# Kernel optimization log

Hardware: AMD Instinct MI355X
Metric: run time of the kernel (lower is better)

## Reference

```python
import jax, jax.numpy as jnp
import numpy as np

STRIDE = 2
PADDING = (1, 1)
OUT_PADDING = (0, 0)


def conv_transpose2d(x, weight, bias, stride, padding, out_padding):
    # weight: (Cin, Cout, kh, kw) -- torch ConvTranspose2d layout.
    # The original code does: stride-insert zeros, zero-pad by (k-1), append
    # out_padding rows/cols, valid-conv with the spatially-flipped kernel,
    # then crop `padding` from each side. That is exactly a dilated conv:
    kh, kw = weight.shape[2], weight.shape[3]
    w = jnp.flip(weight, (2, 3)).transpose(1, 0, 2, 3)  # (Cout, Cin, kh, kw)
    pad = ((kh - 1 - padding[0], kh - 1 - padding[0] + out_padding[0]),
           (kw - 1 - padding[1], kw - 1 - padding[1] + out_padding[1]))
    out = jax.lax.conv_general_dilated(
        x, w,
        window_strides=(1, 1),
        padding=pad,
        lhs_dilation=(stride, stride),
        dimension_numbers=('NCHW', 'OIHW', 'NCHW'))
    return out + bias[None, :, None, None]


def setup_inputs() -> dict:
    key = jax.random.key(0)
    k1, k2, k3 = jax.random.split(key, 3)
    Cin, Cout, kh, kw = 256, 128, 4, 4
    bnd = (1.0 / (Cin * kh * kw)) ** 0.5  # matches uniform_(-k**0.5, k**0.5)
    x = jax.random.normal(k1, (16, Cin, 64, 64), dtype=jnp.float32)
    weight = jax.random.uniform(k2, (Cin, Cout, kh, kw), jnp.float32, -bnd, bnd)
    bias = jax.random.uniform(k3, (Cout,), jnp.float32, -bnd, bnd)
    return {"x": x, "weight": weight, "bias": bias}


def reference(x, weight, bias):
    # Output: (16, 128, 128, 128) = (H-1)*2 - 2*1 + 4
    return conv_transpose2d(x, weight, bias, STRIDE, PADDING, OUT_PADDING)
```

## Files before the change

### kernel.cpp

```cpp
#include <hip/hip_runtime.h>
#include <stdint.h>

typedef unsigned short u16;
typedef __bf16 bf16x8 __attribute__((ext_vector_type(8)));
typedef float f32x4 __attribute__((ext_vector_type(4)));
typedef float f32x2 __attribute__((ext_vector_type(2)));

static const size_t XT_BYTES = (size_t)16 * 66 * 66 * 256 * 2;
static const size_t WK_BYTES = (size_t)2 * 2 * 8 * 2 * 2 * 128 * 32 * 2;

__device__ __forceinline__ u16 f2bf(float f) {
  unsigned u = __float_as_uint(f);
  unsigned r = (u + 0x7fff + ((u >> 16) & 1)) >> 16;
  return (u16)r;
}

__device__ __forceinline__ void ld_g2l16(const u16* g, void* l) {
  __builtin_amdgcn_global_load_lds(
      (const __attribute__((address_space(1))) unsigned int*)(uintptr_t)g,
      (__attribute__((address_space(3))) unsigned int*)(unsigned int)(uintptr_t)l,
      16, 0, 0);
}

__device__ __forceinline__ int swz4(int row) { return (row ^ (row >> 2)) & 3; }

__global__ __launch_bounds__(256) void prep_all(const float* __restrict__ x,
                                                const float* __restrict__ w,
                                                u16* __restrict__ xt,
                                                u16* __restrict__ wk) {
  __shared__ __align__(16) u16 sh[64 * 264];
  const int t = threadIdx.x;
  const int bx = blockIdx.x;
  if (bx >= 1056) {
    int id = (bx - 1056) * 256 + t;
    int ci5 = id & 31;
    int co = (id >> 5) & 127;
    int q = (id >> 12) & 1;
    int dw = (id >> 13) & 1;
    int kc = (id >> 14) & 7;
    int dh = (id >> 17) & 1;
    int p = id >> 18;
    int ci = kc * 32 + ci5;
    int kh = 2 * dh + 1 - p;
    int kw = 2 * dw + 1 - q;
    wk[id] = f2bf(w[((ci * 128 + co) * 4 + kh) * 4 + kw]);
    return;
  }
  const int n = bx / 66;
  const int ihp = bx - n * 66;
  u16* xtn = xt + ((size_t)(n * 66 + ihp)) * 66 * 256;
  if (ihp == 0 || ihp == 65) {
    for (int j = 0; j < 9; ++j) {
      int idx = j * 256 + t;
      if (idx < 2112) ((uint4*)xtn)[idx] = make_uint4(0, 0, 0, 0);
    }
    return;
  }
  const int ih = ihp - 1;
  const int iw0 = (t & 15) * 4;
  const int cb = (t >> 4) * 4;
  const int swz = (t & 3) << 3;
  const float* xb = x + (size_t)n * 1048576 + (size_t)ih * 64 + iw0;
#pragma unroll
  for (int it = 0; it < 4; ++it) {
    int ci0 = it * 64 + cb;
    float4 v0 = *(const float4*)(xb + (size_t)(ci0 + 0) * 4096);
    float4 v1 = *(const float4*)(xb + (size_t)(ci0 + 1) * 4096);
    float4 v2 = *(const float4*)(xb + (size_t)(ci0 + 2) * 4096);
    float4 v3 = *(const float4*)(xb + (size_t)(ci0 + 3) * 4096);
    int col = ci0 ^ swz;
    ushort4 u;
    u.x = f2bf(v0.x); u.y = f2bf(v1.x); u.z = f2bf(v2.x); u.w = f2bf(v3.x);
    *(ushort4*)&sh[(iw0 + 0) * 264 + col] = u;
    u.x = f2bf(v0.y); u.y = f2bf(v1.y); u.z = f2bf(v2.y); u.w = f2bf(v3.y);
    *(ushort4*)&sh[(iw0 + 1) * 264 + col] = u;
    u.x = f2bf(v0.z); u.y = f2bf(v1.z); u.z = f2bf(v2.z); u.w = f2bf(v3.z);
    *(ushort4*)&sh[(iw0 + 2) * 264 + col] = u;
    u.x = f2bf(v0.w); u.y = f2bf(v1.w); u.z = f2bf(v2.w); u.w = f2bf(v3.w);
    *(ushort4*)&sh[(iw0 + 3) * 264 + col] = u;
  }
  __syncthreads();
#pragma unroll
  for (int j = 0; j < 8; ++j) {
    int idx = j * 256 + t;
    int iw = idx >> 5;
    int chunk = idx & 31;
    uint4 v = *(const uint4*)&sh[iw * 264 + ((chunk ^ ((iw >> 2) & 3)) << 3)];
    *(uint4*)&xtn[(size_t)(iw + 1) * 256 + chunk * 8] = v;
  }
  if (t < 64) {
    int iwp = (t >> 5) * 65;
    int chunk = t & 31;
    *(uint4*)&xtn[(size_t)iwp * 256 + chunk * 8] = make_uint4(0, 0, 0, 0);
  }
}

__global__ __launch_bounds__(256, 2) void gemm_ct(const u16* __restrict__ xt,
                                                  const u16* __restrict__ wk,
                                                  const float* __restrict__ bias,
                                                  float* __restrict__ out) {
  __shared__ __align__(16) u16 Bs[2][4224];
  const int t = threadIdx.x;
  const int lane = t & 63;
  const int wv = t >> 6;
  const int wm = wv >> 1, wn = wv & 1;
  const int quad = lane >> 4, l15 = lane & 15;

  const int id = blockIdx.x;
  const int sid = (id & 7) * 128 + (id >> 3);
  const int mt = sid & 31;
  const int n = (sid >> 5) & 15;
  const int p = sid >> 9;
  const int m0 = mt * 2;

  const u16* wka = wk + (size_t)p * 262144 + wm * 2048 + l15 * 32 + quad * 8;
  const u16* xtn = xt + (size_t)n * (66 * 66 * 256);

  int bsrc[3];
#pragma unroll
  for (int it = 0; it < 3; ++it) {
    int c = it * 256 + t;
    int r = (c >= 264) ? 1 : 0;
    int rem = c - 264 * r;
    int iwp = rem >> 2;
    bsrc[it] = r * 16896 + iwp * 256 + ((rem & 3) ^ swz4(iwp)) * 8;
  }

  int bro[3][4];
#pragma unroll
  for (int k = 0; k < 3; ++k)
#pragma unroll
    for (int j = 0; j < 4; ++j) {
      int b0 = j * 16 + l15 + k;
      bro[k][j] = wn * 2112 + b0 * 32 + (quad ^ swz4(b0)) * 8;
    }

  f32x4 acc[2][4][4];
#pragma unroll
  for (int q = 0; q < 2; ++q)
#pragma unroll
    for (int i = 0; i < 4; ++i)
#pragma unroll
      for (int j = 0; j < 4; ++j) acc[q][i][j] = (f32x4){0.f, 0.f, 0.f, 0.f};

  const int mpp1 = m0 + p + 1;

  auto stageB = [&](int buf, int pr) {
    const int kc = pr & 7, dh = pr >> 3;
    const u16* bbase = xtn + (size_t)(mpp1 - dh) * 16896 + kc * 32;
    u16* Bd = &Bs[buf][0];
    ld_g2l16(bbase + bsrc[0], Bd + t * 8);
    ld_g2l16(bbase + bsrc[1], Bd + (256 + t) * 8);
    if (t < 16) ld_g2l16(bbase + bsrc[2], Bd + (512 + t) * 8);
  };

  bf16x8 aC[4], aN[4];
  auto ldA = [&](bf16x8* a, int s, int q) {
    const u16* b = wka + (size_t)s * 8192 + q * 4096;
#pragma unroll
    for (int i = 0; i < 4; ++i) a[i] = *(const bf16x8*)(b + i * 512);
  };

#define MFMA16(ACC, AF, BF)                                              \
  do {                                                                   \
    _Pragma("unroll") for (int i = 0; i < 4; ++i)                        \
        _Pragma("unroll") for (int j = 0; j < 4; ++j)                    \
        ACC[i][j] = __builtin_amdgcn_mfma_f32_16x16x32_bf16(             \
            AF[i], BF[j], ACC[i][j], 0, 0, 0);                           \
  } while (0)

  ldA(aC, 0, 0);
  stageB(0, 0);
  asm volatile("s_waitcnt vmcnt(0)" ::: "memory");
  __builtin_amdgcn_s_barrier();
  asm volatile("" ::: "memory");

  bf16x8 keep[4];
#pragma unroll 1
  for (int pr = 0; pr < 16; ++pr) {
    const u16* Bc = &Bs[pr & 1][0];
    const int s0 = 2 * pr;
    ldA(aN, s0, 1);
    __builtin_amdgcn_sched_barrier(0);
    bf16x8 b2[4];
#pragma unroll
    for (int j = 0; j < 4; ++j) keep[j] = *(const bf16x8*)(Bc + bro[1][j]);
#pragma unroll
    for (int j = 0; j < 4; ++j) b2[j] = *(const bf16x8*)(Bc + bro[2][j]);
    __builtin_amdgcn_s_setprio(1);
    MFMA16(acc[0], aC, keep);
    __builtin_amdgcn_s_setprio(0);
    __builtin_amdgcn_sched_barrier(0);
    ldA(aC, s0 + 1, 0);
    if (pr < 15) stageB((pr + 1) & 1, pr + 1);
    __builtin_amdgcn_sched_barrier(0);
    __builtin_amdgcn_s_setprio(1);
    MFMA16(acc[1], aN, b2);
    __builtin_amdgcn_s_setprio(0);
    __builtin_amdgcn_sched_barrier(0);
    ldA(aN, s0 + 1, 1);
    __builtin_amdgcn_sched_barrier(0);
    bf16x8 b0[4];
#pragma unroll
    for (int j = 0; j < 4; ++j) b0[j] = *(const bf16x8*)(Bc + bro[0][j]);
    __builtin_amdgcn_s_setprio(1);
    MFMA16(acc[0], aC, b0);
    __builtin_amdgcn_s_setprio(0);
    __builtin_amdgcn_sched_barrier(0);
    if (pr < 15) ldA(aC, s0 + 2, 0);
    __builtin_amdgcn_sched_barrier(0);
    __builtin_amdgcn_s_setprio(1);
    MFMA16(acc[1], aN, keep);
    __builtin_amdgcn_s_setprio(0);
    if (pr < 15)
      asm volatile("s_waitcnt lgkmcnt(0) vmcnt(4)" ::: "memory");
    else
      asm volatile("s_waitcnt lgkmcnt(0) vmcnt(0)" ::: "memory");
    __builtin_amdgcn_s_barrier();
    asm volatile("" ::: "memory");
  }
#undef MFMA16

  const int oh = 2 * (m0 + wn) + p;
#pragma unroll
  for (int i = 0; i < 4; ++i) {
#pragma unroll
    for (int j = 0; j < 4; ++j) {
      int l = j * 16 + l15;
#pragma unroll
      for (int r = 0; r < 4; ++r) {
        int co = wm * 64 + i * 16 + quad * 4 + r;
        float bv = bias[co];
        f32x2 v;
        v.x = acc[0][i][j][r] + bv;
        v.y = acc[1][i][j][r] + bv;
        __builtin_nontemporal_store(
            v, (f32x2*)&out[(((size_t)n * 128 + co) * 128 + oh) * 128 + 2 * l]);
      }
    }
  }
}

__global__ __launch_bounds__(256) void ct_fallback(const float* __restrict__ x,
                                                   const float* __restrict__ w,
                                                   const float* __restrict__ bias,
                                                   float* __restrict__ out) {
  size_t id = (size_t)blockIdx.x * 256 + threadIdx.x;
  if (id >= (size_t)16 * 128 * 128 * 128) return;
  int ow = (int)(id & 127), oh = (int)(id >> 7) & 127;
  int co = (int)(id >> 14) & 127, n = (int)(id >> 21);
  int pp = oh & 1, m = oh >> 1, qq = ow & 1, l = ow >> 1;
  float s = bias[co];
  for (int ci = 0; ci < 256; ++ci) {
    for (int dh = 0; dh < 2; ++dh) {
      int ih = m + pp - dh;
      if (ih < 0 || ih > 63) continue;
      int kh = 2 * dh + 1 - pp;
      for (int dw = 0; dw < 2; ++dw) {
        int iw = l + qq - dw;
        if (iw < 0 || iw > 63) continue;
        int kw = 2 * dw + 1 - qq;
        s += x[(((size_t)n * 256 + ci) * 64 + ih) * 64 + iw] *
             w[((ci * 128 + co) * 4 + kh) * 4 + kw];
      }
    }
  }
  out[id] = s;
}

extern "C" void kernel_launch(void* const* d_in, const int* in_sizes, int n_in,
                              void* d_out, int out_size, void* d_ws, size_t ws_size,
                              hipStream_t stream) {
  const float* x = (const float*)d_in[0];
  const float* w = (const float*)d_in[1];
  const float* bias = (const float*)d_in[2];
  float* out = (float*)d_out;
  if (ws_size >= XT_BYTES + WK_BYTES) {
    u16* xt = (u16*)d_ws;
    u16* wkb = (u16*)((char*)d_ws + XT_BYTES);
    hipLaunchKernelGGL(prep_all, dim3(3104), dim3(256), 0, stream, x, w, xt, wkb);
    hipLaunchKernelGGL(gemm_ct, dim3(1024), dim3(256), 0, stream, xt, wkb, bias, out);
  } else {
    hipLaunchKernelGGL(ct_fallback, dim3(131072), dim3(256), 0, stream, x, w, bias, out);
  }
}
```

Measured before the change: 250.8 us.

## Stage weight tiles in LDS and double block size to four output rows

Weight fragments are no longer loaded by each wave straight from global memory into registers. They are now staged through a double-buffered LDS tile using global_load_lds. Blocks grow to 512 threads covering four output rows, so each staged weight tile is shared by more waves and the grid halves. This trades more LDS usage and a full vmcnt(0) wait each iteration, instead of the previous partial wait, for less redundant global weight traffic.

```diff
diff --git a/kernel.cpp b/kernel.cpp
--- a/kernel.cpp
+++ b/kernel.cpp
@@ -95,44 +95,58 @@
   }
 }
 
-__global__ __launch_bounds__(256, 2) void gemm_ct(const u16* __restrict__ xt,
+__global__ __launch_bounds__(512, 2) void gemm_ct(const u16* __restrict__ xt,
                                                   const u16* __restrict__ wk,
                                                   const float* __restrict__ bias,
                                                   float* __restrict__ out) {
-  __shared__ __align__(16) u16 Bs[2][4224];
+  __shared__ __align__(16) u16 As[2][16384];
+  __shared__ __align__(16) u16 Bs[2][8448];
   const int t = threadIdx.x;
   const int lane = t & 63;
   const int wv = t >> 6;
-  const int wm = wv >> 1, wn = wv & 1;
+  const int wm = wv >> 2, wr = wv & 3;
   const int quad = lane >> 4, l15 = lane & 15;
 
   const int id = blockIdx.x;
-  const int sid = (id & 7) * 128 + (id >> 3);
-  const int mt = sid & 31;
-  const int n = (sid >> 5) & 15;
-  const int p = sid >> 9;
-  const int m0 = mt * 2;
-
-  const u16* wka = wk + (size_t)p * 262144 + wm * 2048 + l15 * 32 + quad * 8;
+  const int sid = (id & 7) * 64 + (id >> 3);
+  const int mt = sid & 15;
+  const int n = (sid >> 4) & 15;
+  const int p = sid >> 8;
+  const int m0 = mt * 4;
+
+  const u16* wkp = wk + (size_t)p * 262144;
   const u16* xtn = xt + (size_t)n * (66 * 66 * 256);
 
+  int aoffs[4];
+#pragma unroll
+  for (int it = 0; it < 4; ++it) {
+    int c = it * 512 + t;
+    int rr = c >> 2;
+    aoffs[it] = rr * 32 + ((c & 3) ^ swz4(rr & 127)) * 8;
+  }
   int bsrc[3];
 #pragma unroll
   for (int it = 0; it < 3; ++it) {
-    int c = it * 256 + t;
-    int r = (c >= 264) ? 1 : 0;
-    int rem = c - 264 * r;
+    int c = it * 512 + t;
+    int rr = c / 264;
+    int rem = c - 264 * rr;
     int iwp = rem >> 2;
-    bsrc[it] = r * 16896 + iwp * 256 + ((rem & 3) ^ swz4(iwp)) * 8;
-  }
-
+    bsrc[it] = rr * 16896 + iwp * 256 + ((rem & 3) ^ swz4(iwp)) * 8;
+  }
+
+  int aoff[4];
+#pragma unroll
+  for (int i = 0; i < 4; ++i) {
+    int co = wm * 64 + i * 16 + l15;
+    aoff[i] = co * 32 + (quad ^ swz4(co)) * 8;
+  }
   int bro[3][4];
 #pragma unroll
   for (int k = 0; k < 3; ++k)
 #pragma unroll
     for (int j = 0; j < 4; ++j) {
       int b0 = j * 16 + l15 + k;
-      bro[k][j] = wn * 2112 + b0 * 32 + (quad ^ swz4(b0)) * 8;
+      bro[k][j] = wr * 2112 + b0 * 32 + (quad ^ swz4(b0)) * 8;
     }
 
   f32x4 acc[2][4][4];
@@ -143,22 +157,18 @@
 #pragma unroll
       for (int j = 0; j < 4; ++j) acc[q][i][j] = (f32x4){0.f, 0.f, 0.f, 0.f};
 
-  const int mpp1 = m0 + p + 1;
-
-  auto stageB = [&](int buf, int pr) {
+  auto stage = [&](int buf, int pr) {
     const int kc = pr & 7, dh = pr >> 3;
-    const u16* bbase = xtn + (size_t)(mpp1 - dh) * 16896 + kc * 32;
+    const u16* asrc = wkp + (size_t)(dh * 8 + kc) * 16384;
+    u16* Ad = &As[buf][0];
+#pragma unroll
+    for (int it = 0; it < 4; ++it)
+      ld_g2l16(asrc + aoffs[it], Ad + (it * 512 + t) * 8);
+    const u16* bbase = xtn + (size_t)(m0 + p - dh + 1) * 16896 + kc * 32;
     u16* Bd = &Bs[buf][0];
     ld_g2l16(bbase + bsrc[0], Bd + t * 8);
-    ld_g2l16(bbase + bsrc[1], Bd + (256 + t) * 8);
-    if (t < 16) ld_g2l16(bbase + bsrc[2], Bd + (512 + t) * 8);
-  };
-
-  bf16x8 aC[4], aN[4];
-  auto ldA = [&](bf16x8* a, int s, int q) {
-    const u16* b = wka + (size_t)s * 8192 + q * 4096;
-#pragma unroll
-    for (int i = 0; i < 4; ++i) a[i] = *(const bf16x8*)(b + i * 512);
+    ld_g2l16(bbase + bsrc[1], Bd + (512 + t) * 8);
+    if (t < 32) ld_g2l16(bbase + bsrc[2], Bd + (1024 + t) * 8);
   };
 
 #define MFMA16(ACC, AF, BF)                                              \
@@ -169,59 +179,54 @@
             AF[i], BF[j], ACC[i][j], 0, 0, 0);                           \
   } while (0)
 
-  ldA(aC, 0, 0);
-  stageB(0, 0);
+  stage(0, 0);
   asm volatile("s_waitcnt vmcnt(0)" ::: "memory");
   __builtin_amdgcn_s_barrier();
   asm volatile("" ::: "memory");
 
-  bf16x8 keep[4];
-#pragma unroll 1
+#pragma unroll 2
   for (int pr = 0; pr < 16; ++pr) {
+    const u16* Ac = &As[pr & 1][0];
     const u16* Bc = &Bs[pr & 1][0];
-    const int s0 = 2 * pr;
-    ldA(aN, s0, 1);
-    __builtin_amdgcn_sched_barrier(0);
-    bf16x8 b2[4];
+    if (pr < 15) stage((pr + 1) & 1, pr + 1);
+    __builtin_amdgcn_sched_barrier(0);
+    bf16x8 keep[4], bx[4], af[4];
 #pragma unroll
     for (int j = 0; j < 4; ++j) keep[j] = *(const bf16x8*)(Bc + bro[1][j]);
 #pragma unroll
-    for (int j = 0; j < 4; ++j) b2[j] = *(const bf16x8*)(Bc + bro[2][j]);
-    __builtin_amdgcn_s_setprio(1);
-    MFMA16(acc[0], aC, keep);
-    __builtin_amdgcn_s_setprio(0);
-    __builtin_amdgcn_sched_barrier(0);
-    ldA(aC, s0 + 1, 0);
-    if (pr < 15) stageB((pr + 1) & 1, pr + 1);
-    __builtin_amdgcn_sched_barrier(0);
-    __builtin_amdgcn_s_setprio(1);
-    MFMA16(acc[1], aN, b2);
-    __builtin_amdgcn_s_setprio(0);
-    __builtin_amdgcn_sched_barrier(0);
-    ldA(aN, s0 + 1, 1);
-    __builtin_amdgcn_sched_barrier(0);
-    bf16x8 b0[4];
-#pragma unroll
-    for (int j = 0; j < 4; ++j) b0[j] = *(const bf16x8*)(Bc + bro[0][j]);
-    __builtin_amdgcn_s_setprio(1);
-    MFMA16(acc[0], aC, b0);
-    __builtin_amdgcn_s_setprio(0);
-    __builtin_amdgcn_sched_barrier(0);
-    if (pr < 15) ldA(aC, s0 + 2, 0);
-    __builtin_amdgcn_sched_barrier(0);
-    __builtin_amdgcn_s_setprio(1);
-    MFMA16(acc[1], aN, keep);
-    __builtin_amdgcn_s_setprio(0);
-    if (pr < 15)
-      asm volatile("s_waitcnt lgkmcnt(0) vmcnt(4)" ::: "memory");
-    else
-      asm volatile("s_waitcnt lgkmcnt(0) vmcnt(0)" ::: "memory");
+    for (int i = 0; i < 4; ++i) af[i] = *(const bf16x8*)(Ac + aoff[i]);
+    __builtin_amdgcn_s_setprio(1);
+    MFMA16(acc[0], af, keep);
+    __builtin_amdgcn_s_setprio(0);
+    __builtin_amdgcn_sched_barrier(0);
+#pragma unroll
+    for (int j = 0; j < 4; ++j) bx[j] = *(const bf16x8*)(Bc + bro[2][j]);
+#pragma unroll
+    for (int i = 0; i < 4; ++i) af[i] = *(const bf16x8*)(Ac + 4096 + aoff[i]);
+    __builtin_amdgcn_s_setprio(1);
+    MFMA16(acc[1], af, bx);
+    __builtin_amdgcn_s_setprio(0);
+    __builtin_amdgcn_sched_barrier(0);
+#pragma unroll
+    for (int j = 0; j < 4; ++j) bx[j] = *(const bf16x8*)(Bc + bro[0][j]);
+#pragma unroll
+    for (int i = 0; i < 4; ++i) af[i] = *(const bf16x8*)(Ac + 8192 + aoff[i]);
+    __builtin_amdgcn_s_setprio(1);
+    MFMA16(acc[0], af, bx);
+    __builtin_amdgcn_s_setprio(0);
+    __builtin_amdgcn_sched_barrier(0);
+#pragma unroll
+    for (int i = 0; i < 4; ++i) af[i] = *(const bf16x8*)(Ac + 12288 + aoff[i]);
+    __builtin_amdgcn_s_setprio(1);
+    MFMA16(acc[1], af, keep);
+    __builtin_amdgcn_s_setprio(0);
+    asm volatile("s_waitcnt lgkmcnt(0) vmcnt(0)" ::: "memory");
     __builtin_amdgcn_s_barrier();
     asm volatile("" ::: "memory");
   }
 #undef MFMA16
 
-  const int oh = 2 * (m0 + wn) + p;
+  const int oh = 2 * (m0 + wr) + p;
 #pragma unroll
   for (int i = 0; i < 4; ++i) {
 #pragma unroll
@@ -279,7 +284,7 @@
     u16* xt = (u16*)d_ws;
     u16* wkb = (u16*)((char*)d_ws + XT_BYTES);
     hipLaunchKernelGGL(prep_all, dim3(3104), dim3(256), 0, stream, x, w, xt, wkb);
-    hipLaunchKernelGGL(gemm_ct, dim3(1024), dim3(256), 0, stream, xt, wkb, bias, out);
+    hipLaunchKernelGGL(gemm_ct, dim3(512), dim3(512), 0, stream, xt, wkb, bias, out);
   } else {
     hipLaunchKernelGGL(ct_fallback, dim3(131072), dim3(256), 0, stream, x, w, bias, out);
   }
```

After: 241.6 us. -3.7%, faster.
